# Performance work log

Hardware: AMD Instinct MI355X
Metric: run time of the kernel (lower is better)

## Reference

```python
import jax, jax.numpy as jnp
import numpy as np

_CLIP_MIN = 1e-6
_POS_ALPHA = 1e-3
RADIUS = 3
HALF_D = RADIUS * RADIUS  # 9: patch vector length per class
N_FINE, N_MID, N_HIGH = 19, 7, 3
LAMBDA = 0.5
LOSS_WEIGHT = 1.0
IGNORE = 255

_F2M = np.array([0,0,0,1,1,1,2,2,3,3,4,5,5,6,6,6,6,6,6], dtype=np.int64)
_M2H = np.array([0,0,1,1,1,2,2], dtype=np.int64)
_F2H = _M2H[_F2M]


def setup_inputs():
    key = jax.random.key(0)
    k1, k2, k3, k4 = jax.random.split(key, 4)
    B, H, W, D = 4, 512, 512, 256
    return {
        "step": 5000,
        "embedding": jax.random.normal(k1, (B, D, H // 8, W // 8), jnp.float32),
        "cls_score_before": jax.random.normal(k2, (B, N_FINE, H // 8, W // 8), jnp.float32),
        "cls_score": jax.random.normal(k3, (B, N_FINE + N_MID + N_HIGH, H, W), jnp.float32),
        "label": jax.random.randint(k4, (B, H, W), 0, N_FINE),
        "fine_to_mid": jnp.asarray(_F2M),
        "fine_to_high": jnp.asarray(_F2H),
    }


def _maxpool3(x):  # kernel=stride=3, VALID (rmi_pool_way=0)
    return jax.lax.reduce_window(x, -jnp.inf, jax.lax.max, (1, 1, 3, 3), (1, 1, 3, 3), "VALID")


def _map_get_pairs(la, pr, radius=RADIUS):
    b, c, h, w = la.shape
    nh, nw = h - radius + 1, w - radius + 1
    las = [la[:, :, y:y + nh, x:x + nw] for y in range(radius) for x in range(radius)]
    prs = [pr[:, :, y:y + nh, x:x + nw] for y in range(radius) for x in range(radius)]
    la_v = jnp.stack(las, axis=2).reshape(b, c, radius * radius, nh * nw)
    pr_v = jnp.stack(prs, axis=2).reshape(b, c, radius * radius, nh * nw)
    return la_v, pr_v


def _rmi_lower_bound(oh, probs, vmask):
    # oh, probs: [B,C,H,W]; vmask: [B,1,H,W]
    la = _maxpool3(oh * vmask)
    pr = _maxpool3(probs * vmask + _CLIP_MIN)
    la_v, pr_v = _map_get_pairs(la, pr)  # [B,C,half_d,N]
    la_v = jax.lax.stop_gradient(la_v)   # labels are detached in the original
    la_v = la_v - la_v.mean(axis=-1, keepdims=True)
    pr_v = pr_v - pr_v.mean(axis=-1, keepdims=True)
    diag = _POS_ALPHA * jnp.eye(HALF_D, dtype=la_v.dtype)
    pr_cov = jnp.einsum("bcdn,bcen->bcde", pr_v, pr_v) + diag
    la_cov = jnp.einsum("bcdn,bcen->bcde", la_v, la_v)
    la_pr = jnp.einsum("bcdn,bcen->bcde", la_v, pr_v)
    appro = la_cov - la_pr @ jnp.linalg.solve(pr_cov, jnp.swapaxes(la_pr, -1, -2)) + diag
    chol = jnp.linalg.cholesky(appro)
    logdet = 2.0 * jnp.sum(jnp.log(jnp.diagonal(chol, axis1=-2, axis2=-1) + 1e-8), axis=-1)  # [B,C]
    return jnp.sum(logdet.mean(axis=0) / HALF_D)


def _hiera_bce(oh, pos, neg, vmask):
    # positives judged against min-combined probs, negatives against max-combined probs
    loss = -(oh * jnp.log(pos + 1e-8) + (1.0 - oh) * jnp.log(1.0 - neg + 1e-8)) * vmask
    return loss.sum() / (vmask.sum() * oh.shape[1] + 1e-8)


def _forward(cls_score, label, fine_to_mid, fine_to_high):
    probs = jax.nn.sigmoid(cls_score.astype(jnp.float32))
    valid = (label != IGNORE)
    vmask = valid[:, None].astype(jnp.float32)  # [B,1,H,W]
    lf = jnp.where(valid, label, 0)
    lm = fine_to_mid[lf]
    lh = fine_to_high[lf]
    oh_f = jax.nn.one_hot(lf, N_FINE, axis=1, dtype=jnp.float32)
    oh_m = jax.nn.one_hot(lm, N_MID, axis=1, dtype=jnp.float32)
    oh_h = jax.nn.one_hot(lh, N_HIGH, axis=1, dtype=jnp.float32)
    MCMA = probs[:, :N_FINE]
    MCMB = probs[:, N_FINE:N_FINE + N_MID]
    MCMC = probs[:, N_FINE + N_MID:]
    # upward (max) hierarchy consistency
    segf = jax.ops.segment_max(jnp.moveaxis(MCMA, 1, 0), fine_to_mid, num_segments=N_MID)
    MCMB_c = jnp.maximum(jnp.moveaxis(segf, 0, 1), MCMB)
    mid_to_high = jnp.zeros((N_MID,), dtype=fine_to_high.dtype).at[fine_to_mid].set(fine_to_high)
    segm = jax.ops.segment_max(jnp.moveaxis(MCMB_c, 1, 0), mid_to_high, num_segments=N_HIGH)
    MCMC_c = jnp.maximum(jnp.moveaxis(segm, 0, 1), MCMC)
    # downward (min) hierarchy consistency
    MCLA = jnp.minimum(MCMA, MCMB[:, fine_to_mid])
    MCLB_c = jnp.minimum(MCMB, MCMC[:, mid_to_high])
    MCLC_c = MCMC
    total = 0.0
    for oh, pos, neg in ((oh_f, MCLA, MCMA), (oh_m, MCLB_c, MCMB_c), (oh_h, MCLC_c, MCMC_c)):
        bce = _hiera_bce(oh, pos, neg, vmask)
        rmi = _rmi_lower_bound(oh, pos, vmask)
        total = total + LAMBDA * bce + (1.0 - LAMBDA) * rmi
    return LOSS_WEIGHT * total


def reference(step, embedding, cls_score_before, cls_score, label, fine_to_mid, fine_to_high):
    # step / embedding / cls_score_before feed only the triplet branch (not in provided source)
    return _forward(cls_score, label, fine_to_mid, fine_to_high)
```

## Files before the change

### kernel.cpp

```cpp
#include <hip/hip_runtime.h>
#include <math.h>

namespace {
constexpr int NB = 4, NCHT = 29, NF = 19, NM = 7, NHI = 3;
constexpr int HH = 512, WW = 512;
constexpr int PH  = 170;
constexpr int NHW = 168;
constexpr int NS  = NHW * NHW;
constexpr int NBC = NB * NCHT;
constexpr int CROWS = 14;
constexpr int NCH2  = NHW / CROWS;

constexpr int F2M[NF] = {0,0,0,1,1,1,2,2,3,3,4,5,5,6,6,6,6,6,6};
constexpr int M2H[NM] = {0,0,1,1,1,2,2};
constexpr int F2H[NF] = {0,0,0,0,0,0,1,1,1,1,1,2,2,2,2,2,2,2,2};

constexpr unsigned long long packTbl(const int* a, int n) {
  unsigned long long p = 0;
  for (int i = 0; i < n; i++) p |= (unsigned long long)(a[i]) << (3 * i);
  return p;
}
constexpr unsigned long long PF2M = packTbl(F2M, NF);
constexpr unsigned long long PF2H = packTbl(F2H, NF);

constexpr int    WS_S1  = 16;
constexpr int    WS_COV = 4096;
constexpr int    WS_RED = 49152;
constexpr size_t WS_LA  = 65536;
constexpr size_t WS_PR  = WS_LA + (size_t)NBC * PH * PH;
constexpr size_t WS_ZERO_BYTES = (size_t)(WS_RED + 64 * 16) * 4;
}

#define GLOAD16(gsrc, ldst)                                                     \
  __builtin_amdgcn_global_load_lds(                                             \
      (const __attribute__((address_space(1))) void*)(gsrc),                    \
      (__attribute__((address_space(3))) void*)(ldst), 16, 0, 0)

__global__ __launch_bounds__(256, 4)
void kA(const float* __restrict__ cls, const int* __restrict__ label,
        float* __restrict__ ws) {
  const int bx  = blockIdx.x;
  const int wy  = blockIdx.y;
  const int b   = blockIdx.z;
  const int tid = threadIdx.x;
  const int x0  = 96 * bx;
  const int y0  = 3 * wy;
  const int rmax = (wy == 170) ? 1 : 2;

  const int W4   = (bx < 5) ? 24 : 8;
  const int NCOL = 4 * W4;
  const int CST  = 3 * NCOL;
  const int NW   = (bx < 5) ? 32 : 10;

  __shared__ __align__(16) float    sPixF[NCHT * 288];
  __shared__ __align__(16) int      sLbl[288];
  __shared__ unsigned sMask[288];
  __shared__ float    sRed[4][4];

  {
    const int T3 = 3 * W4;
    const int total = NCHT * T3;
    for (int i = tid; i < total; i += 256) {
      const int c   = i / T3;
      const int rem = i - c * T3;
      const int r   = rem / W4;
      const int f   = rem - r * W4;
      const int rr  = (r <= rmax) ? r : rmax;
      const float* src =
          cls + ((size_t)(b * NCHT + c) * HH + (y0 + rr)) * WW + x0 + 4 * f;
      GLOAD16(src, &sPixF[4 * i]);
    }
    for (int i = tid; i < T3; i += 256) {
      const int r  = i / W4;
      const int f  = i - r * W4;
      const int rr = (r <= rmax) ? r : rmax;
      const int* src = label + ((size_t)b * HH + (y0 + rr)) * WW + x0 + 4 * f;
      GLOAD16(src, &sLbl[4 * i]);
    }
  }
  __syncthreads();

  float bce0 = 0.f, bce1 = 0.f, bce2 = 0.f, cnt = 0.f;
  for (int p = tid; p < CST; p += 256) {
    const int r = p / NCOL;
    if (r <= rmax) {
      const int lbl = sLbl[p];
      const bool valid = (lbl != 255);
      const int lf = valid ? lbl : 0;
      const int lm = (int)((PF2M >> (3 * lf)) & 7ull);
      const int lh = (int)((PF2H >> (3 * lf)) & 7ull);
      const float vm = valid ? 1.f : 0.f;

      float pv[NCHT];
      #pragma unroll
      for (int c = 0; c < NCHT; c++)
        pv[c] = __builtin_amdgcn_rcpf(1.f + __expf(-sPixF[c * CST + p]));

      float segf[NM];
      #pragma unroll
      for (int m = 0; m < NM; m++) segf[m] = -1.f;
      #pragma unroll
      for (int f = 0; f < NF; f++) segf[F2M[f]] = fmaxf(segf[F2M[f]], pv[f]);
      float pBc[NM];
      #pragma unroll
      for (int m = 0; m < NM; m++) pBc[m] = fmaxf(segf[m], pv[NF + m]);
      float segm[NHI];
      #pragma unroll
      for (int k = 0; k < NHI; k++) segm[k] = -1.f;
      #pragma unroll
      for (int m = 0; m < NM; m++) segm[M2H[m]] = fmaxf(segm[M2H[m]], pBc[m]);
      float pCc[NHI];
      #pragma unroll
      for (int k = 0; k < NHI; k++) pCc[k] = fmaxf(segm[k], pv[NF + NM + k]);

      #pragma unroll
      for (int f = 0; f < NF; f++) {
        const float pos = fminf(pv[f], pv[NF + F2M[f]]);
        if (valid)
          bce0 -= __logf((f == lf) ? pos + 1e-8f : 1.f - pv[f] + 1e-8f);
        sPixF[f * CST + p] = pos * vm + 1e-6f;
      }
      #pragma unroll
      for (int m = 0; m < NM; m++) {
        const float pos = fminf(pv[NF + m], pv[NF + NM + M2H[m]]);
        if (valid)
          bce1 -= __logf((m == lm) ? pos + 1e-8f : 1.f - pBc[m] + 1e-8f);
        sPixF[(NF + m) * CST + p] = pos * vm + 1e-6f;
      }
      #pragma unroll
      for (int k = 0; k < NHI; k++) {
        const float pos = pv[NF + NM + k];
        if (valid)
          bce2 -= __logf((k == lh) ? pos + 1e-8f : 1.f - pCc[k] + 1e-8f);
        sPixF[(NF + NM + k) * CST + p] = pos * vm + 1e-6f;
      }
      sMask[p] = valid ? ((1u << lf) | (1u << (19 + lm)) | (1u << (26 + lh))) : 0u;
      cnt += vm;
    }
  }

  #pragma unroll
  for (int m = 32; m >= 1; m >>= 1) {
    bce0 += __shfl_xor(bce0, m);
    bce1 += __shfl_xor(bce1, m);
    bce2 += __shfl_xor(bce2, m);
    cnt  += __shfl_xor(cnt, m);
  }
  {
    const int wave = tid >> 6, lane = tid & 63;
    if (lane == 0) {
      sRed[0][wave] = bce0; sRed[1][wave] = bce1;
      sRed[2][wave] = bce2; sRed[3][wave] = cnt;
    }
  }
  __syncthreads();

  if (wy < 170 && tid < NW) {
    const int wx = 32 * bx + tid;
    const int c0 = 3 * tid;
    float* la = ws + WS_LA;
    float* pr = ws + WS_PR;
    unsigned m = 0u;
    #pragma unroll
    for (int r = 0; r < 3; r++)
      m |= sMask[r * NCOL + c0] | sMask[r * NCOL + c0 + 1] | sMask[r * NCOL + c0 + 2];
    const size_t base = ((size_t)(b * NCHT) * PH + wy) * PH + wx;
    #pragma unroll
    for (int c = 0; c < NF; c++)
      la[base + (size_t)c * PH * PH] = (float)((m >> c) & 1u);
    #pragma unroll
    for (int mm = 0; mm < NM; mm++)
      la[base + (size_t)(NF + mm) * PH * PH] = (float)((m >> (19 + mm)) & 1u);
    #pragma unroll
    for (int k = 0; k < NHI; k++)
      la[base + (size_t)(NF + NM + k) * PH * PH] = (float)((m >> (26 + k)) & 1u);
    #pragma unroll
    for (int c = 0; c < NCHT; c++) {
      float v = 0.f;
      #pragma unroll
      for (int r = 0; r < 3; r++)
        v = fmaxf(v, fmaxf(fmaxf(sPixF[c * CST + r * NCOL + c0],
                                 sPixF[c * CST + r * NCOL + c0 + 1]),
                           sPixF[c * CST + r * NCOL + c0 + 2]));
      pr[base + (size_t)c * PH * PH] = v;
    }
  }

  if (tid == 0) {
    const int slot = (bx + 6 * (wy + 171 * b)) & 63;
    float* dst = ws + WS_RED + slot * 16;
    atomicAdd(&dst[0], sRed[0][0] + sRed[0][1] + sRed[0][2] + sRed[0][3]);
    atomicAdd(&dst[1], sRed[1][0] + sRed[1][1] + sRed[1][2] + sRed[1][3]);
    atomicAdd(&dst[2], sRed[2][0] + sRed[2][1] + sRed[2][2] + sRed[2][3]);
    atomicAdd(&dst[3], sRed[3][0] + sRed[3][1] + sRed[3][2] + sRed[3][3]);
  }
}

__global__ __launch_bounds__(192)
void kCov(const float* __restrict__ ws_base, float* __restrict__ cov,
          float* __restrict__ s1out) {
  const int bc    = blockIdx.x / NCH2;
  const int chunk = blockIdx.x % NCH2;
  const int tid   = threadIdx.x;
  const int tile  = tid / 32;
  const int g     = tid % 32;
  const int ta = (tile < 3) ? 0 : ((tile < 5) ? 1 : 2);
  const int tb = (tile < 3) ? tile : ((tile < 5) ? tile - 2 : 2);
  const bool diag = (ta == tb);

  __shared__ __align__(16) float sA[16 * PH];
  __shared__ __align__(16) float sP[16 * PH];

  const int r0 = chunk * CROWS;
  const float* Ag = ws_base + WS_LA + (size_t)bc * PH * PH + (size_t)r0 * PH;
  const float* Pg = ws_base + WS_PR + (size_t)bc * PH * PH + (size_t)r0 * PH;
  for (int i = tid; i < (16 * PH) / 4; i += 192) {
    GLOAD16(Ag + 4 * i, &sA[4 * i]);
    GLOAD16(Pg + 4 * i, &sP[4 * i]);
  }
  __syncthreads();

  const float* baseA[6];
  const float* baseB[6];
  #pragma unroll
  for (int k = 0; k < 6; k++) {
    int r = 6 * ta + k, rr = r % 9;
    baseA[k] = ((r < 9) ? sA : sP) + (rr / 3) * PH + (rr % 3);
    int r2 = 6 * tb + k, rr2 = r2 % 9;
    baseB[k] = ((r2 < 9) ? sA : sP) + (rr2 / 3) * PH + (rr2 % 3);
  }

  float acc[6][6];
  #pragma unroll
  for (int k = 0; k < 6; k++)
    #pragma unroll
    for (int l = 0; l < 6; l++) acc[k][l] = 0.f;
  float sums[6];
  #pragma unroll
  for (int k = 0; k < 6; k++) sums[k] = 0.f;

  for (int lr = 0; lr < CROWS; lr++) {
    const int rowoff = lr * PH;
    for (int lc = g; lc < NHW; lc += 32) {
      float va[6], vb[6];
      #pragma unroll
      for (int k = 0; k < 6; k++) va[k] = baseA[k][rowoff + lc];
      #pragma unroll
      for (int k = 0; k < 6; k++) vb[k] = baseB[k][rowoff + lc];
      #pragma unroll
      for (int k = 0; k < 6; k++)
        #pragma unroll
        for (int l = 0; l < 6; l++) acc[k][l] = fmaf(va[k], vb[l], acc[k][l]);
      if (diag) {
        #pragma unroll
        for (int k = 0; k < 6; k++) sums[k] += va[k];
      }
    }
  }

  #pragma unroll
  for (int k = 0; k < 6; k++)
    #pragma unroll
    for (int l = 0; l < 6; l++) {
      float v = acc[k][l];
      #pragma unroll
      for (int m = 16; m >= 1; m >>= 1) v += __shfl_xor(v, m);
      acc[k][l] = v;
    }
  if (diag) {
    #pragma unroll
    for (int k = 0; k < 6; k++) {
      float v = sums[k];
      #pragma unroll
      for (int m = 16; m >= 1; m >>= 1) v += __shfl_xor(v, m);
      sums[k] = v;
    }
  }
  if (g == 0) {
    float* dst = cov + (size_t)bc * 324;
    #pragma unroll
    for (int k = 0; k < 6; k++)
      #pragma unroll
      for (int l = 0; l < 6; l++)
        atomicAdd(&dst[(6 * ta + k) * 18 + 6 * tb + l], acc[k][l]);
    if (diag) {
      #pragma unroll
      for (int k = 0; k < 6; k++)
        atomicAdd(&s1out[bc * 32 + 6 * ta + k], sums[k]);
    }
  }
}

__global__ __launch_bounds__(64)
void kSolve(const float* __restrict__ cov_all, const float* __restrict__ s1,
            float* __restrict__ acc) {
  const int bc   = blockIdx.x;
  const int lane = threadIdx.x;
  const float* cr = cov_all + (size_t)bc * 324;
  const double n = (double)NS;

  double mu[18];
  #pragma unroll
  for (int r = 0; r < 18; r++) mu[r] = (double)s1[bc * 32 + r] / n;
#define CC(i, j) ((double)cr[(i) * 18 + (j)] - n * mu[(i)] * mu[(j)])

  double row[9];
  #pragma unroll
  for (int j = 0; j < 9; j++)
    row[j] = (lane < 9 && j <= lane) ? CC(9 + j, 9 + lane) : 0.0;
  if (lane < 9) row[lane] += 1e-3;

  #pragma unroll
  for (int k = 0; k < 9; k++) {
    if (lane == k) {
      double s = row[k];
      #pragma unroll
      for (int m = 0; m < k; m++) s -= row[m] * row[m];
      row[k] = sqrt(fmax(s, 1e-300));
    }
    double rk[9];
    #pragma unroll
    for (int m = 0; m <= k; m++) rk[m] = __shfl(row[m], k);
    if (lane > k && lane < 9) {
      double s = row[k];
      #pragma unroll
      for (int m = 0; m < k; m++) s -= row[m] * rk[m];
      row[k] = s / rk[k];
    }
  }

  double Lm[9][9];
  #pragma unroll
  for (int i = 0; i < 9; i++)
    #pragma unroll
    for (int m = 0; m <= i; m++) Lm[i][m] = __shfl(row[m], i);

  double mc[9];
  #pragma unroll
  for (int r = 0; r < 9; r++) mc[r] = 0.0;
  if (lane < 9) {
    #pragma unroll
    for (int r = 0; r < 9; r++) {
      double s = CC(lane, 9 + r);
      #pragma unroll
      for (int m = 0; m < r; m++) s -= Lm[r][m] * mc[m];
      mc[r] = s / Lm[r][r];
    }
  }

  double a2[9];
  #pragma unroll
  for (int j = 0; j < 9; j++) a2[j] = 0.0;
  #pragma unroll
  for (int j = 0; j < 9; j++) {
    double mj[9];
    #pragma unroll
    for (int r = 0; r < 9; r++) mj[r] = __shfl(mc[r], j);
    double dot = 0.0;
    #pragma unroll
    for (int r = 0; r < 9; r++) dot += mc[r] * mj[r];
    if (lane < 9 && j <= lane)
      a2[j] = CC(j, lane) - dot + ((j == lane) ? 1e-3 : 0.0);
  }
#undef CC

  double myld = 0.0;
  #pragma unroll
  for (int k = 0; k < 9; k++) {
    if (lane == k) {
      double s = a2[k];
      #pragma unroll
      for (int m = 0; m < k; m++) s -= a2[m] * a2[m];
      double d = sqrt(fmax(s, 0.0));
      a2[k] = d;
      myld = 2.0 * log(d + 1e-8);
    }
    double rk[9];
    #pragma unroll
    for (int m = 0; m <= k; m++) rk[m] = __shfl(a2[m], k);
    if (lane > k && lane < 9) {
      double s = a2[k];
      #pragma unroll
      for (int m = 0; m < k; m++) s -= a2[m] * rk[m];
      a2[k] = s / rk[k];
    }
  }
  #pragma unroll
  for (int m = 32; m >= 1; m >>= 1) myld += __shfl_xor(myld, m);
  if (lane == 0) atomicAdd(&acc[4], (float)myld);
}

__global__ void kFin(const float* __restrict__ ws, float* __restrict__ out) {
  const int tid = threadIdx.x;
  const float* slot = ws + WS_RED + tid * 16;
  float b0 = slot[0], b1 = slot[1], b2 = slot[2], b3 = slot[3];
  #pragma unroll
  for (int m = 32; m >= 1; m >>= 1) {
    b0 += __shfl_xor(b0, m);
    b1 += __shfl_xor(b1, m);
    b2 += __shfl_xor(b2, m);
    b3 += __shfl_xor(b3, m);
  }
  if (tid == 0) {
    const double cnt = (double)b3;
    const double bce = 0.5 * ((double)b0 / (cnt * NF + 1e-8) +
                              (double)b1 / (cnt * NM + 1e-8) +
                              (double)b2 / (cnt * NHI + 1e-8));
    const double rmi = 0.5 * (double)ws[4] / (double)(NB * 9);
    out[0] = (float)(bce + rmi);
  }
}

extern "C" void kernel_launch(void* const* d_in, const int* in_sizes, int n_in,
                              void* d_out, int out_size, void* d_ws, size_t ws_size,
                              hipStream_t stream) {
  (void)in_sizes; (void)n_in; (void)out_size; (void)ws_size;
  const float* cls   = (const float*)d_in[3];
  const int*   label = (const int*)d_in[4];
  float* ws = (float*)d_ws;

  hipMemsetAsync(d_ws, 0, WS_ZERO_BYTES, stream);

  dim3 gA(6, 171, NB);
  kA<<<gA, 256, 0, stream>>>(cls, label, ws);
  kCov<<<NBC * NCH2, 192, 0, stream>>>(ws, ws + WS_COV, ws + WS_S1);
  kSolve<<<NBC, 64, 0, stream>>>(ws + WS_COV, ws + WS_S1, ws);
  kFin<<<1, 64, 0, stream>>>(ws, (float*)d_out);
}
```

Baseline: 135.7 us.

## Widen kA to 320 threads, one pixel per thread, parallelize pooled writes

Raises the kA block size to 320 threads so each thread handles at most one pixel (CST max 288), which removes the per-pixel loop. The label staging into LDS is dropped and labels are read straight from global memory. The pooled-window output stage now uses 8 threads per window, each striding over the channels, instead of one thread writing all 29 channels serially. The trade-off is lower occupancy, since the launch bound no longer asks for 4 blocks per CU, and uncoalesced or extra label loads.

```diff
diff --git a/kernel.cpp b/kernel.cpp
--- a/kernel.cpp
+++ b/kernel.cpp
@@ -36,7 +36,7 @@
       (const __attribute__((address_space(1))) void*)(gsrc),                    \
       (__attribute__((address_space(3))) void*)(ldst), 16, 0, 0)
 
-__global__ __launch_bounds__(256, 4)
+__global__ __launch_bounds__(320)
 void kA(const float* __restrict__ cls, const int* __restrict__ label,
         float* __restrict__ ws) {
   const int bx  = blockIdx.x;
@@ -53,14 +53,13 @@
   const int NW   = (bx < 5) ? 32 : 10;
 
   __shared__ __align__(16) float    sPixF[NCHT * 288];
-  __shared__ __align__(16) int      sLbl[288];
   __shared__ unsigned sMask[288];
-  __shared__ float    sRed[4][4];
+  __shared__ float    sRed[4][5];
 
   {
     const int T3 = 3 * W4;
     const int total = NCHT * T3;
-    for (int i = tid; i < total; i += 256) {
+    for (int i = tid; i < total; i += 320) {
       const int c   = i / T3;
       const int rem = i - c * T3;
       const int r   = rem / W4;
@@ -70,21 +69,16 @@
           cls + ((size_t)(b * NCHT + c) * HH + (y0 + rr)) * WW + x0 + 4 * f;
       GLOAD16(src, &sPixF[4 * i]);
     }
-    for (int i = tid; i < T3; i += 256) {
-      const int r  = i / W4;
-      const int f  = i - r * W4;
-      const int rr = (r <= rmax) ? r : rmax;
-      const int* src = label + ((size_t)b * HH + (y0 + rr)) * WW + x0 + 4 * f;
-      GLOAD16(src, &sLbl[4 * i]);
-    }
   }
   __syncthreads();
 
   float bce0 = 0.f, bce1 = 0.f, bce2 = 0.f, cnt = 0.f;
-  for (int p = tid; p < CST; p += 256) {
+  {
+    const int p = tid;
     const int r = p / NCOL;
-    if (r <= rmax) {
-      const int lbl = sLbl[p];
+    if (p < CST && r <= rmax) {
+      const int col = p - r * NCOL;
+      const int lbl = label[((size_t)b * HH + (y0 + r)) * WW + x0 + col];
       const bool valid = (lbl != 255);
       const int lf = valid ? lbl : 0;
       const int lm = (int)((PF2M >> (3 * lf)) & 7ull);
@@ -135,7 +129,7 @@
         sPixF[(NF + NM + k) * CST + p] = pos * vm + 1e-6f;
       }
       sMask[p] = valid ? ((1u << lf) | (1u << (19 + lm)) | (1u << (26 + lh))) : 0u;
-      cnt += vm;
+      cnt = vm;
     }
   }
 
@@ -155,27 +149,19 @@
   }
   __syncthreads();
 
-  if (wy < 170 && tid < NW) {
-    const int wx = 32 * bx + tid;
-    const int c0 = 3 * tid;
+  if (wy < 170 && tid < 8 * NW) {
+    const int w = tid >> 3;
+    const int s = tid & 7;
+    const int c0 = 3 * w;
     float* la = ws + WS_LA;
     float* pr = ws + WS_PR;
     unsigned m = 0u;
     #pragma unroll
     for (int r = 0; r < 3; r++)
       m |= sMask[r * NCOL + c0] | sMask[r * NCOL + c0 + 1] | sMask[r * NCOL + c0 + 2];
-    const size_t base = ((size_t)(b * NCHT) * PH + wy) * PH + wx;
-    #pragma unroll
-    for (int c = 0; c < NF; c++)
+    const size_t base = ((size_t)(b * NCHT) * PH + wy) * PH + (32 * bx + w);
+    for (int c = s; c < NCHT; c += 8) {
       la[base + (size_t)c * PH * PH] = (float)((m >> c) & 1u);
-    #pragma unroll
-    for (int mm = 0; mm < NM; mm++)
-      la[base + (size_t)(NF + mm) * PH * PH] = (float)((m >> (19 + mm)) & 1u);
-    #pragma unroll
-    for (int k = 0; k < NHI; k++)
-      la[base + (size_t)(NF + NM + k) * PH * PH] = (float)((m >> (26 + k)) & 1u);
-    #pragma unroll
-    for (int c = 0; c < NCHT; c++) {
       float v = 0.f;
       #pragma unroll
       for (int r = 0; r < 3; r++)
@@ -189,10 +175,10 @@
   if (tid == 0) {
     const int slot = (bx + 6 * (wy + 171 * b)) & 63;
     float* dst = ws + WS_RED + slot * 16;
-    atomicAdd(&dst[0], sRed[0][0] + sRed[0][1] + sRed[0][2] + sRed[0][3]);
-    atomicAdd(&dst[1], sRed[1][0] + sRed[1][1] + sRed[1][2] + sRed[1][3]);
-    atomicAdd(&dst[2], sRed[2][0] + sRed[2][1] + sRed[2][2] + sRed[2][3]);
-    atomicAdd(&dst[3], sRed[3][0] + sRed[3][1] + sRed[3][2] + sRed[3][3]);
+    atomicAdd(&dst[0], sRed[0][0] + sRed[0][1] + sRed[0][2] + sRed[0][3] + sRed[0][4]);
+    atomicAdd(&dst[1], sRed[1][0] + sRed[1][1] + sRed[1][2] + sRed[1][3] + sRed[1][4]);
+    atomicAdd(&dst[2], sRed[2][0] + sRed[2][1] + sRed[2][2] + sRed[2][3] + sRed[2][4]);
+    atomicAdd(&dst[3], sRed[3][0] + sRed[3][1] + sRed[3][2] + sRed[3][3] + sRed[3][4]);
   }
 }
 
@@ -422,7 +408,7 @@
   hipMemsetAsync(d_ws, 0, WS_ZERO_BYTES, stream);
 
   dim3 gA(6, 171, NB);
-  kA<<<gA, 256, 0, stream>>>(cls, label, ws);
+  kA<<<gA, 320, 0, stream>>>(cls, label, ws);
   kCov<<<NBC * NCH2, 192, 0, stream>>>(ws, ws + WS_COV, ws + WS_S1);
   kSolve<<<NBC, 64, 0, stream>>>(ws + WS_COV, ws + WS_S1, ws);
   kFin<<<1, 64, 0, stream>>>(ws, (float*)d_out);
```

After: 138.9 us. +2.4%, slower.
